# Kernel optimization log

Hardware: AMD Instinct MI355X
Metric: run time of the kernel (lower is better)

## Reference

```python
import jax, jax.numpy as jnp
import numpy as np

EPS = 1e-9       # module's displacement/convergence epsilon
COS_EPS = 1e-8   # torch F.cosine_similarity eps (norms clamped at eps)
LN_EPS = 1e-5


def _safe_norm(sq):
    # sqrt with zero-safe gradient for exactly-zero (padded) vectors
    return jnp.where(sq > 0, jnp.sqrt(jnp.maximum(sq, 1e-30)), 0.0)


def _features(coords, n):
    """coords: [S, md] padded; n: true length (>=4). Returns [60] features."""
    S, md = coords.shape
    f32 = coords.dtype
    nf = n.astype(f32)
    idx_d = jnp.arange(S - 1)
    m = n - 1                       # number of valid deltas
    mf = m.astype(f32)
    dmask = idx_d < m
    dmaskf = dmask.astype(f32)

    deltas = (coords[1:] - coords[:-1]) * dmaskf[:, None]     # [S-1, md]
    dmags = _safe_norm(jnp.sum(deltas * deltas, axis=-1))      # [S-1]

    last = jnp.take(coords, n - 1, axis=0)
    total_disp = _safe_norm(jnp.sum((last - coords[0]) ** 2))
    path_len = jnp.sum(dmags)
    disp_ratio = total_disp / (path_len + EPS)
    n_steps_norm = nf / 10.0

    # consecutive cosine similarities / curvatures (valid count = n-2)
    na = jnp.maximum(dmags, COS_EPS)
    cos = jnp.sum(deltas[:-1] * deltas[1:], axis=-1) / (na[:-1] * na[1:])  # [S-2]
    idx_c = jnp.arange(S - 2)
    cmask = idx_c < (n - 2)
    cmaskf = cmask.astype(f32)
    ncf = (n - 2).astype(f32)
    curv = 1.0 - cos
    curv_m = jnp.where(cmask, curv, 0.0)
    mean_curv = jnp.sum(curv_m) / ncf
    max_curv = jnp.max(jnp.where(cmask, curv, -jnp.inf))
    min_curv = jnp.min(jnp.where(cmask, curv, jnp.inf))
    curv_var = jnp.sum(cmaskf * (curv - mean_curv) ** 2) / jnp.maximum(ncf - 1.0, 1.0)
    std_curv = jnp.where(ncf > 1.0, jnp.sqrt(jnp.maximum(curv_var, 1e-30)), 0.0)
    curv_range = max_curv - min_curv

    mean_cos = jnp.sum(jnp.where(cmask, cos, 0.0)) / ncf
    min_cos = jnp.min(jnp.where(cmask, cos, jnp.inf))
    dir_changes = jnp.sum(cmaskf * (cos < 0).astype(f32)) / jnp.maximum(ncf, 1.0)

    linearity = disp_ratio
    loop_score = 1.0 - total_disp / (path_len + EPS)

    half = m // 2
    fmaskf = (idx_d < half + 1).astype(f32)
    smaskf = ((idx_d >= half) & (idx_d < m)).astype(f32)
    first_half = jnp.sum(dmags * fmaskf) / (half + 1).astype(f32)
    second_half = jnp.sum(dmags * smaskf) / (m - half).astype(f32)
    convergence = (first_half - second_half) / (first_half + EPS)
    cascade = (second_half - first_half) / (first_half + EPS)

    # all-pairs cosine (the O(n^2) block) via one GEMM per sample
    cosmat = (deltas @ deltas.T) / (na[:, None] * na[None, :])  # [S-1, S-1]
    pmask = (idx_d[:, None] < idx_d[None, :]) & (idx_d[None, :] < m)
    npairs = mf * (mf - 1.0) / 2.0
    parallelism = jnp.sum(jnp.where(pmask, cosmat, 0.0)) / jnp.maximum(npairs, 1.0)

    mean_dm = path_len / mf
    dm_var = jnp.sum(dmaskf * (dmags - mean_dm) ** 2) / jnp.maximum(mf - 1.0, 1.0)
    std_dm = jnp.where(mf > 1.0, jnp.sqrt(jnp.maximum(dm_var, 1e-30)), 0.0)
    max_dm = jnp.max(jnp.where(dmask, dmags, -jnp.inf))
    jump = jnp.where(mean_dm > EPS, max_dm / mean_dm, 1.0)

    rmaskf = (jnp.arange(S) < n).astype(f32)
    cnt = nf * md
    mean_coord = jnp.sum(coords * rmaskf[:, None]) / cnt
    coord_var = jnp.sum(rmaskf[:, None] * (coords - mean_coord) ** 2) / (cnt - 1.0)
    std_coord = jnp.sqrt(jnp.maximum(coord_var, 1e-30))

    scalars = jnp.stack([
        total_disp, path_len, disp_ratio, n_steps_norm,
        mean_curv, max_curv, std_curv, curv_range,
        mean_cos, min_cos, dir_changes,
        linearity, loop_score, convergence, parallelism, jump, cascade,
        mean_dm, std_dm, mean_coord, std_coord,
    ])  # [21]
    padded_deltas = deltas[:3].reshape(-1)   # [30] (masked -> already zero-padded)
    padded_curvs = curv_m[:9]                # [9]
    return jnp.concatenate([scalars, padded_deltas, padded_curvs])  # [60]


def setup_inputs() -> dict:
    key = jax.random.key(0)
    ks = jax.random.split(key, 4)
    B, S, md, H = 32768, 48, 10, 48
    coords = jax.random.normal(ks[0], (B, S, md), dtype=jnp.float32)
    lengths = jax.random.randint(ks[1], (B,), 4, S + 1, dtype=jnp.int32)
    W = jax.random.normal(ks[2], (60, H), dtype=jnp.float32) * 0.1
    b = jax.random.normal(ks[3], (H,), dtype=jnp.float32) * 0.01
    ln_w = jnp.ones((H,), dtype=jnp.float32)
    ln_b = jnp.zeros((H,), dtype=jnp.float32)
    return {"coords": coords, "lengths": lengths, "W": W, "b": b, "ln_w": ln_w, "ln_b": ln_b}


def reference(coords, lengths, W, b, ln_w, ln_b):
    feats = jax.vmap(_features)(coords, lengths)          # [B, 60]
    h = feats @ W + b                                     # [B, 48]
    mu = jnp.mean(h, axis=-1, keepdims=True)
    var = jnp.mean((h - mu) ** 2, axis=-1, keepdims=True)
    h = (h - mu) / jnp.sqrt(var + LN_EPS) * ln_w + ln_b
    return jax.nn.gelu(h, approximate=False)              # dropout is identity at eval
```

## Files before the change

kernel.cpp:

```cpp
#include <hip/hip_runtime.h>
#include <math.h>

#define WPB 4

template<int CTRL, int RM>
static __device__ __forceinline__ float dppadd(float x){
  int t = __builtin_amdgcn_update_dpp(0, __float_as_int(x), CTRL, RM, 0xf, true);
  return x + __int_as_float(t);
}
template<int CTRL, int RM>
static __device__ __forceinline__ float dppmax(float x){
  int t = __builtin_amdgcn_update_dpp(__float_as_int(x), __float_as_int(x), CTRL, RM, 0xf, false);
  return fmaxf(x, __int_as_float(t));
}
template<int CTRL, int RM>
static __device__ __forceinline__ float dppmin(float x){
  int t = __builtin_amdgcn_update_dpp(__float_as_int(x), __float_as_int(x), CTRL, RM, 0xf, false);
  return fminf(x, __int_as_float(t));
}
static __device__ __forceinline__ float rl(float x, int l){
  return __uint_as_float(__builtin_amdgcn_readlane(__float_as_uint(x), l));
}
static __device__ __forceinline__ float wsum(float x){
  x = dppadd<0x111,0xf>(x);
  x = dppadd<0x112,0xf>(x);
  x = dppadd<0x114,0xf>(x);
  x = dppadd<0x118,0xf>(x);
  x = dppadd<0x142,0xa>(x);
  x = dppadd<0x143,0xc>(x);
  return rl(x, 63);
}
static __device__ __forceinline__ float wmax(float x){
  x = dppmax<0x111,0xf>(x); x = dppmax<0x112,0xf>(x);
  x = dppmax<0x114,0xf>(x); x = dppmax<0x118,0xf>(x);
  x = dppmax<0x142,0xa>(x); x = dppmax<0x143,0xc>(x);
  return rl(x, 63);
}
static __device__ __forceinline__ float wmin(float x){
  x = dppmin<0x111,0xf>(x); x = dppmin<0x112,0xf>(x);
  x = dppmin<0x114,0xf>(x); x = dppmin<0x118,0xf>(x);
  x = dppmin<0x142,0xa>(x); x = dppmin<0x143,0xc>(x);
  return rl(x, 63);
}
static __device__ __forceinline__ float frcp(float x){ return __builtin_amdgcn_rcpf(x); }
static __device__ __forceinline__ float fsqrt(float x){ return __builtin_amdgcn_sqrtf(x); }

__global__ void transpose_w(const float* __restrict__ W, float* __restrict__ Wt){
  int idx = blockIdx.x * 256 + threadIdx.x;
  if (idx < 60 * 48) { int f = idx / 48, j = idx - f * 48; Wt[j * 60 + f] = W[idx]; }
}

template<bool USEWT>
__global__ __launch_bounds__(WPB * 64)
void traj_kernel(const float* __restrict__ coords,
                 const int* __restrict__ lengths,
                 const float* __restrict__ Wsrc,
                 const float* __restrict__ bias,
                 const float* __restrict__ lnw,
                 const float* __restrict__ lnb,
                 float* __restrict__ out, int B)
{
  const int i = threadIdx.x & 63;
  const int b = blockIdx.x * WPB + (threadIdx.x >> 6);
  if (b >= B) return;

  const int n = __builtin_amdgcn_readfirstlane(lengths[b]);
  const int m = n - 1;
  const float* cp = coords + (size_t)b * 480;

  float c[10], cnx[10];
  if (i < 48) {
    const float2* p = reinterpret_cast<const float2*>(cp + i * 10);
    float2 v0 = p[0], v1 = p[1], v2 = p[2], v3 = p[3], v4 = p[4];
    c[0]=v0.x; c[1]=v0.y; c[2]=v1.x; c[3]=v1.y; c[4]=v2.x;
    c[5]=v2.y; c[6]=v3.x; c[7]=v3.y; c[8]=v4.x; c[9]=v4.y;
  } else {
#pragma unroll
    for (int k = 0; k < 10; k++) c[k] = 0.f;
  }
  if (i < 47) {
    const float2* p = reinterpret_cast<const float2*>(cp + (i + 1) * 10);
    float2 v0 = p[0], v1 = p[1], v2 = p[2], v3 = p[3], v4 = p[4];
    cnx[0]=v0.x; cnx[1]=v0.y; cnx[2]=v1.x; cnx[3]=v1.y; cnx[4]=v2.x;
    cnx[5]=v2.y; cnx[6]=v3.x; cnx[7]=v3.y; cnx[8]=v4.x; cnx[9]=v4.y;
  } else {
#pragma unroll
    for (int k = 0; k < 10; k++) cnx[k] = 0.f;
  }

  const bool dact = (i < m);
  float d[10]; float dsq = 0.f;
#pragma unroll
  for (int k = 0; k < 10; k++) {
    float dd = dact ? (cnx[k] - c[k]) : 0.f;
    d[k] = dd;
    dsq = fmaf(dd, dd, dsq);
  }
  const float dmag = (dsq > 0.f) ? fsqrt(fmaxf(dsq, 1e-30f)) : 0.f;
  const float na   = fmaxf(dmag, 1e-8f);
  const float inv  = frcp(na);

  float dot = 0.f;
#pragma unroll
  for (int k = 0; k < 10; k++) {
    float dn = __shfl_down(d[k], 1, 64);
    dot = fmaf(d[k], dn, dot);
  }
  const float invn = __shfl_down(inv, 1, 64);
  const bool cact = (i < n - 2);
  const float cosv  = dot * inv * invn;
  const float cos_m = cact ? cosv : 0.f;

  const int half = m >> 1;
  const float path_len = wsum(dmag);
  const float sum_dm2  = wsum(dsq);
  const float max_dm   = wmax(dmag);
  const float sum_f    = wsum((i <= half) ? dmag : 0.f);
  const float dm_half  = __uint_as_float(__builtin_amdgcn_readlane(__float_as_uint(dmag), half));
  const float sum_s    = path_len + dm_half - sum_f;

  const float sum_cos  = wsum(cos_m);
  const float sum_cos2 = wsum(cos_m * cos_m);
  const float max_cos  = wmax(cact ? cosv : -INFINITY);
  const float min_cos  = wmin(cact ? cosv :  INFINITY);
  const float sum_ng   = wsum((cact && cosv < 0.f) ? 1.f : 0.f);

  float Usq = 0.f;
#pragma unroll
  for (int k = 0; k < 10; k++) {
    float Uk = wsum(d[k] * inv);
    Usq = fmaf(Uk, Uk, Usq);
  }
  const float sum_uu = wsum(dsq * (inv * inv));

  float csl = 0.f, cs2l = 0.f;
  if (i < n) {
#pragma unroll
    for (int k = 0; k < 10; k++) { csl += c[k]; cs2l = fmaf(c[k], c[k], cs2l); }
  }
  const float sum_c  = wsum(csl);
  const float sum_c2 = wsum(cs2l);

  float tsql = 0.f;
#pragma unroll
  for (int k = 0; k < 10; k++) {
    float c0 = rl(c[k], 0);
    float t = c[k] - c0;
    tsql = fmaf(t, t, tsql);
  }
  const float tdq = __uint_as_float(__builtin_amdgcn_readlane(__float_as_uint(tsql), m));
  const float total_disp = (tdq > 0.f) ? fsqrt(fmaxf(tdq, 1e-30f)) : 0.f;

  const float EPSf = 1e-9f;
  const float nf = (float)n, mf = (float)m, ncf = (float)(n - 2);
  const float rncf = frcp(ncf);
  const float disp_ratio = total_disp * frcp(path_len + EPSf);
  const float sum_cv  = ncf - sum_cos;
  const float mean_cv = sum_cv * rncf;
  const float sum_cv2 = fmaf(-2.f, sum_cos, ncf) + sum_cos2;
  const float cv_var  = (sum_cv2 - ncf * mean_cv * mean_cv) * frcp(fmaxf(ncf - 1.f, 1.f));
  const float std_cv  = fsqrt(fmaxf(cv_var, 1e-30f));
  const float max_cv  = 1.f - min_cos;
  const float cv_rng  = max_cos - min_cos;
  const float mean_cs = sum_cos * rncf;
  const float dirchg  = sum_ng * rncf;
  const float fh = sum_f * frcp((float)(half + 1));
  const float sh = sum_s * frcp((float)(m - half));
  const float conv = (fh - sh) * frcp(fh + EPSf);
  const float npairs = mf * (mf - 1.f) * 0.5f;
  const float par = (Usq - sum_uu) * 0.5f * frcp(npairs);
  const float mean_dm = path_len * frcp(mf);
  const float dm_var = (sum_dm2 - mf * mean_dm * mean_dm) * frcp(mf - 1.f);
  const float std_dm = fsqrt(fmaxf(dm_var, 1e-30f));
  const float jump = (mean_dm > EPSf) ? max_dm * frcp(mean_dm) : 1.f;
  const float cnt = nf * 10.f;
  const float mean_co = sum_c * frcp(cnt);
  const float co_var = (sum_c2 - cnt * mean_co * mean_co) * frcp(cnt - 1.f);
  const float std_co = fsqrt(fmaxf(co_var, 1e-30f));

  float feat[60];
  feat[0]  = total_disp;
  feat[1]  = path_len;
  feat[2]  = disp_ratio;
  feat[3]  = nf * 0.1f;
  feat[4]  = mean_cv;
  feat[5]  = max_cv;
  feat[6]  = std_cv;
  feat[7]  = cv_rng;
  feat[8]  = mean_cs;
  feat[9]  = min_cos;
  feat[10] = dirchg;
  feat[11] = disp_ratio;
  feat[12] = 1.f - disp_ratio;
  feat[13] = conv;
  feat[14] = par;
  feat[15] = jump;
  feat[16] = -conv;
  feat[17] = mean_dm;
  feat[18] = std_dm;
  feat[19] = mean_co;
  feat[20] = std_co;
#pragma unroll
  for (int r = 0; r < 3; r++)
#pragma unroll
    for (int k = 0; k < 10; k++)
      feat[21 + r * 10 + k] = rl(d[k], r);
  const float curv_m = cact ? (1.f - cosv) : 0.f;
#pragma unroll
  for (int r = 0; r < 9; r++)
    feat[51 + r] = rl(curv_m, r);

  float h = 0.f;
  if (i < 48) {
    h = bias[i];
    if (USEWT) {
      const float4* wr = reinterpret_cast<const float4*>(Wsrc + i * 60);
#pragma unroll
      for (int q = 0; q < 15; ++q) {
        float4 w = wr[q];
        h = fmaf(feat[4 * q + 0], w.x, h);
        h = fmaf(feat[4 * q + 1], w.y, h);
        h = fmaf(feat[4 * q + 2], w.z, h);
        h = fmaf(feat[4 * q + 3], w.w, h);
      }
    } else {
#pragma unroll
      for (int f = 0; f < 60; ++f) h = fmaf(feat[f], Wsrc[f * 48 + i], h);
    }
  }

  const float hm = (i < 48) ? h : 0.f;
  const float s1 = wsum(hm);
  const float s2 = wsum(hm * hm);
  const float mu  = s1 * (1.f / 48.f);
  const float var = fmaf(-mu, mu, s2 * (1.f / 48.f));

  if (i < 48) {
    float x = (h - mu) * __builtin_amdgcn_rsqf(var + 1e-5f) * lnw[i] + lnb[i];
    float g = 0.5f * x * (1.f + erff(x * 0.70710678118654752f));
    out[(size_t)b * 48 + i] = g;
  }
}

extern "C" void kernel_launch(void* const* d_in, const int* in_sizes, int n_in,
                              void* d_out, int out_size, void* d_ws, size_t ws_size,
                              hipStream_t stream)
{
  const float* coords = (const float*)d_in[0];
  const int*   lengths= (const int*)d_in[1];
  const float* W      = (const float*)d_in[2];
  const float* bias   = (const float*)d_in[3];
  const float* lnw    = (const float*)d_in[4];
  const float* lnb    = (const float*)d_in[5];
  float* out = (float*)d_out;

  const int B = in_sizes[1];
  const int blocks = (B + WPB - 1) / WPB;

  if (ws_size >= (size_t)(60 * 48 * sizeof(float))) {
    float* Wt = (float*)d_ws;
    transpose_w<<<12, 256, 0, stream>>>(W, Wt);
    traj_kernel<true><<<blocks, WPB * 64, 0, stream>>>(coords, lengths, Wt, bias, lnw, lnb, out, B);
  } else {
    traj_kernel<false><<<blocks, WPB * 64, 0, stream>>>(coords, lengths, W, bias, lnw, lnb, out, B);
  }
}
```

Baseline: 126.4 us.

## Process four trajectories per wavefront with 16-lane reductions and tanh GELU

Maps each trajectory to a 16-lane group, with each lane handling three rows, instead of one trajectory per 64-lane wavefront. Reductions shrink to 16-lane DPP plus a swizzle broadcast, and neighbour deltas for the cosine terms are reloaded from memory rather than shuffled across lanes. This is meant to remove idle lanes and cut the cost of the many full-wave reductions. It also replaces the exact erf GELU with the tanh approximation via exp2, which adds small numerical differences, and the extra per-lane arrays raise register pressure.

```diff
diff --git a/kernel.cpp b/kernel.cpp
--- a/kernel.cpp
+++ b/kernel.cpp
@@ -1,49 +1,40 @@
 #include <hip/hip_runtime.h>
 #include <math.h>
 
-#define WPB 4
-
-template<int CTRL, int RM>
+static __device__ __forceinline__ float frcp(float x){ return __builtin_amdgcn_rcpf(x); }
+static __device__ __forceinline__ float fsq (float x){ return __builtin_amdgcn_sqrtf(x); }
+
+template<int CTRL>
 static __device__ __forceinline__ float dppadd(float x){
-  int t = __builtin_amdgcn_update_dpp(0, __float_as_int(x), CTRL, RM, 0xf, true);
+  int t = __builtin_amdgcn_update_dpp(0, __float_as_int(x), CTRL, 0xf, 0xf, true);
   return x + __int_as_float(t);
 }
-template<int CTRL, int RM>
+template<int CTRL>
 static __device__ __forceinline__ float dppmax(float x){
-  int t = __builtin_amdgcn_update_dpp(__float_as_int(x), __float_as_int(x), CTRL, RM, 0xf, false);
+  int t = __builtin_amdgcn_update_dpp(__float_as_int(x), __float_as_int(x), CTRL, 0xf, 0xf, false);
   return fmaxf(x, __int_as_float(t));
 }
-template<int CTRL, int RM>
+template<int CTRL>
 static __device__ __forceinline__ float dppmin(float x){
-  int t = __builtin_amdgcn_update_dpp(__float_as_int(x), __float_as_int(x), CTRL, RM, 0xf, false);
+  int t = __builtin_amdgcn_update_dpp(__float_as_int(x), __float_as_int(x), CTRL, 0xf, 0xf, false);
   return fminf(x, __int_as_float(t));
 }
-static __device__ __forceinline__ float rl(float x, int l){
-  return __uint_as_float(__builtin_amdgcn_readlane(__float_as_uint(x), l));
-}
-static __device__ __forceinline__ float wsum(float x){
-  x = dppadd<0x111,0xf>(x);
-  x = dppadd<0x112,0xf>(x);
-  x = dppadd<0x114,0xf>(x);
-  x = dppadd<0x118,0xf>(x);
-  x = dppadd<0x142,0xa>(x);
-  x = dppadd<0x143,0xc>(x);
-  return rl(x, 63);
-}
-static __device__ __forceinline__ float wmax(float x){
-  x = dppmax<0x111,0xf>(x); x = dppmax<0x112,0xf>(x);
-  x = dppmax<0x114,0xf>(x); x = dppmax<0x118,0xf>(x);
-  x = dppmax<0x142,0xa>(x); x = dppmax<0x143,0xc>(x);
-  return rl(x, 63);
-}
-static __device__ __forceinline__ float wmin(float x){
-  x = dppmin<0x111,0xf>(x); x = dppmin<0x112,0xf>(x);
-  x = dppmin<0x114,0xf>(x); x = dppmin<0x118,0xf>(x);
-  x = dppmin<0x142,0xa>(x); x = dppmin<0x143,0xc>(x);
-  return rl(x, 63);
-}
-static __device__ __forceinline__ float frcp(float x){ return __builtin_amdgcn_rcpf(x); }
-static __device__ __forceinline__ float fsqrt(float x){ return __builtin_amdgcn_sqrtf(x); }
+static __device__ __forceinline__ float rsum16(float x){
+  x = dppadd<0x111>(x); x = dppadd<0x112>(x);
+  x = dppadd<0x114>(x); x = dppadd<0x118>(x);
+  return __int_as_float(__builtin_amdgcn_ds_swizzle(__float_as_int(x), 0x1F0));
+}
+static __device__ __forceinline__ float rmax16(float x){
+  x = dppmax<0x111>(x); x = dppmax<0x112>(x);
+  x = dppmax<0x114>(x); x = dppmax<0x118>(x);
+  return __int_as_float(__builtin_amdgcn_ds_swizzle(__float_as_int(x), 0x1F0));
+}
+static __device__ __forceinline__ float rmin16(float x){
+  x = dppmin<0x111>(x); x = dppmin<0x112>(x);
+  x = dppmin<0x114>(x); x = dppmin<0x118>(x);
+  return __int_as_float(__builtin_amdgcn_ds_swizzle(__float_as_int(x), 0x1F0));
+}
+#define BC(P, x) __int_as_float(__builtin_amdgcn_ds_swizzle(__float_as_int(x), 0x10 | ((P) << 5)))
 
 __global__ void transpose_w(const float* __restrict__ W, float* __restrict__ Wt){
   int idx = blockIdx.x * 256 + threadIdx.x;
@@ -51,7 +42,7 @@
 }
 
 template<bool USEWT>
-__global__ __launch_bounds__(WPB * 64)
+__global__ __launch_bounds__(256)
 void traj_kernel(const float* __restrict__ coords,
                  const int* __restrict__ lengths,
                  const float* __restrict__ Wsrc,
@@ -60,96 +51,142 @@
                  const float* __restrict__ lnb,
                  float* __restrict__ out, int B)
 {
-  const int i = threadIdx.x & 63;
-  const int b = blockIdx.x * WPB + (threadIdx.x >> 6);
-  if (b >= B) return;
-
-  const int n = __builtin_amdgcn_readfirstlane(lengths[b]);
+  const int lane = threadIdx.x & 63;
+  const int s    = lane & 15;
+  const int grp  = (blockIdx.x * 4 + (threadIdx.x >> 6)) * 4 + (lane >> 4);
+  const bool bvalid = (grp < B);
+  const int b = bvalid ? grp : (B - 1);
+
+  const int n = lengths[b];
   const int m = n - 1;
   const float* cp = coords + (size_t)b * 480;
 
-  float c[10], cnx[10];
-  if (i < 48) {
-    const float2* p = reinterpret_cast<const float2*>(cp + i * 10);
-    float2 v0 = p[0], v1 = p[1], v2 = p[2], v3 = p[3], v4 = p[4];
-    c[0]=v0.x; c[1]=v0.y; c[2]=v1.x; c[3]=v1.y; c[4]=v2.x;
-    c[5]=v2.y; c[6]=v3.x; c[7]=v3.y; c[8]=v4.x; c[9]=v4.y;
-  } else {
-#pragma unroll
-    for (int k = 0; k < 10; k++) c[k] = 0.f;
-  }
-  if (i < 47) {
-    const float2* p = reinterpret_cast<const float2*>(cp + (i + 1) * 10);
-    float2 v0 = p[0], v1 = p[1], v2 = p[2], v3 = p[3], v4 = p[4];
-    cnx[0]=v0.x; cnx[1]=v0.y; cnx[2]=v1.x; cnx[3]=v1.y; cnx[4]=v2.x;
-    cnx[5]=v2.y; cnx[6]=v3.x; cnx[7]=v3.y; cnx[8]=v4.x; cnx[9]=v4.y;
-  } else {
-#pragma unroll
-    for (int k = 0; k < 10; k++) cnx[k] = 0.f;
-  }
-
-  const bool dact = (i < m);
-  float d[10]; float dsq = 0.f;
-#pragma unroll
-  for (int k = 0; k < 10; k++) {
-    float dd = dact ? (cnx[k] - c[k]) : 0.f;
-    d[k] = dd;
-    dsq = fmaf(dd, dd, dsq);
-  }
-  const float dmag = (dsq > 0.f) ? fsqrt(fmaxf(dsq, 1e-30f)) : 0.f;
-  const float na   = fmaxf(dmag, 1e-8f);
-  const float inv  = frcp(na);
-
-  float dot = 0.f;
-#pragma unroll
-  for (int k = 0; k < 10; k++) {
-    float dn = __shfl_down(d[k], 1, 64);
-    dot = fmaf(d[k], dn, dot);
-  }
-  const float invn = __shfl_down(inv, 1, 64);
-  const bool cact = (i < n - 2);
-  const float cosv  = dot * inv * invn;
-  const float cos_m = cact ? cosv : 0.f;
+  float c[3][10], cn[3][10];
+#pragma unroll
+  for (int q = 0; q < 3; ++q) {
+    const float2* p = reinterpret_cast<const float2*>(cp + (q * 16 + s) * 10);
+#pragma unroll
+    for (int k = 0; k < 5; ++k) { float2 v = p[k]; c[q][2*k] = v.x; c[q][2*k+1] = v.y; }
+  }
+#pragma unroll
+  for (int q = 0; q < 3; ++q) {
+    const int row = q * 16 + s + 1;
+    if (row < 48) {
+      const float2* p = reinterpret_cast<const float2*>(cp + row * 10);
+#pragma unroll
+      for (int k = 0; k < 5; ++k) { float2 v = p[k]; cn[q][2*k] = v.x; cn[q][2*k+1] = v.y; }
+    } else {
+#pragma unroll
+      for (int k = 0; k < 10; ++k) cn[q][k] = 0.f;
+    }
+  }
+
+  float csl = 0.f, cs2l = 0.f;
+#pragma unroll
+  for (int q = 0; q < 3; ++q) {
+    float t1 = 0.f, t2 = 0.f;
+#pragma unroll
+    for (int k = 0; k < 10; ++k) { t1 += c[q][k]; t2 = fmaf(c[q][k], c[q][k], t2); }
+    const bool act = (q * 16 + s) < n;
+    csl  += act ? t1 : 0.f;
+    cs2l += act ? t2 : 0.f;
+  }
+  const float sum_c  = rsum16(csl);
+  const float sum_c2 = rsum16(cs2l);
+
+  float cc0[10];
+#pragma unroll
+  for (int k = 0; k < 10; ++k) cc0[k] = BC(0, c[0][k]);
+  const int qs = (n - 1) >> 4, ssl = (n - 1) & 15;
+  float tql = 0.f;
+#pragma unroll
+  for (int q = 0; q < 3; ++q) {
+    float tq = 0.f;
+#pragma unroll
+    for (int k = 0; k < 10; ++k) { float t = c[q][k] - cc0[k]; tq = fmaf(t, t, tq); }
+    tql = (s == ssl && q == qs) ? tq : tql;
+  }
+  const float tdq = rsum16(tql);
+  const float total_disp = (tdq > 0.f) ? fsq(fmaxf(tdq, 1e-30f)) : 0.f;
 
   const int half = m >> 1;
-  const float path_len = wsum(dmag);
-  const float sum_dm2  = wsum(dsq);
-  const float max_dm   = wmax(dmag);
-  const float sum_f    = wsum((i <= half) ? dmag : 0.f);
-  const float dm_half  = __uint_as_float(__builtin_amdgcn_readlane(__float_as_uint(dmag), half));
-  const float sum_s    = path_len + dm_half - sum_f;
-
-  const float sum_cos  = wsum(cos_m);
-  const float sum_cos2 = wsum(cos_m * cos_m);
-  const float max_cos  = wmax(cact ? cosv : -INFINITY);
-  const float min_cos  = wmin(cact ? cosv :  INFINITY);
-  const float sum_ng   = wsum((cact && cosv < 0.f) ? 1.f : 0.f);
-
+  float d[3][10], inv[3];
+  float path_l=0.f, dm2_l=0.f, maxdm_l=0.f, sf_l=0.f, ss_l=0.f, uu_l=0.f;
+  float uk[10];
+#pragma unroll
+  for (int k = 0; k < 10; ++k) uk[k] = 0.f;
+#pragma unroll
+  for (int q = 0; q < 3; ++q) {
+    const int j = q * 16 + s;
+    float ds_ = 0.f;
+#pragma unroll
+    for (int k = 0; k < 10; ++k) { float dd = cn[q][k] - c[q][k]; d[q][k] = dd; ds_ = fmaf(dd, dd, ds_); }
+    const float sn = (ds_ > 0.f) ? fsq(fmaxf(ds_, 1e-30f)) : 0.f;
+    inv[q] = frcp(fmaxf(sn, 1e-8f));
+    const bool jm = j < m;
+    const float dm = jm ? sn : 0.f;
+    path_l += dm;
+    dm2_l  += jm ? ds_ : 0.f;
+    maxdm_l = fmaxf(maxdm_l, dm);
+    sf_l += (j <= half) ? dm : 0.f;
+    ss_l += (j >= half) ? dm : 0.f;
+    const float invm = jm ? inv[q] : 0.f;
+#pragma unroll
+    for (int k = 0; k < 10; ++k) uk[k] = fmaf(d[q][k], invm, uk[k]);
+    uu_l = fmaf(ds_ * invm, invm, uu_l);
+  }
+
+  const int rotb = (((lane & 48) | ((lane + 1) & 15)) << 2);
+  const float rinv0 = __int_as_float(__builtin_amdgcn_ds_bpermute(rotb, __float_as_int(inv[0])));
+  const float rinv1 = __int_as_float(__builtin_amdgcn_ds_bpermute(rotb, __float_as_int(inv[1])));
+  const float rinv2 = __int_as_float(__builtin_amdgcn_ds_bpermute(rotb, __float_as_int(inv[2])));
+  float invn[3];
+  invn[0] = (s < 15) ? rinv0 : rinv1;
+  invn[1] = (s < 15) ? rinv1 : rinv2;
+  invn[2] = (s < 15) ? rinv2 : 0.f;
+
+  float cos_l=0.f, cos2_l=0.f, ng_l=0.f, maxc_l=-INFINITY, minc_l=INFINITY;
+  float curv0 = 0.f;
+#pragma unroll
+  for (int q = 0; q < 3; ++q) {
+    const int j = q * 16 + s;
+    float dn[10];
+    if (j + 2 < 48) {
+      const float2* p = reinterpret_cast<const float2*>(cp + (j + 2) * 10);
+#pragma unroll
+      for (int k = 0; k < 5; ++k) { float2 v = p[k]; dn[2*k] = v.x - cn[q][2*k]; dn[2*k+1] = v.y - cn[q][2*k+1]; }
+    } else {
+#pragma unroll
+      for (int k = 0; k < 10; ++k) dn[k] = 0.f;
+    }
+    float dot = 0.f;
+#pragma unroll
+    for (int k = 0; k < 10; ++k) dot = fmaf(d[q][k], dn[k], dot);
+    const float cosv = dot * inv[q] * invn[q];
+    const bool ca = j < (n - 2);
+    const float cm = ca ? cosv : 0.f;
+    cos_l += cm;
+    cos2_l = fmaf(cm, cm, cos2_l);
+    maxc_l = fmaxf(maxc_l, ca ? cosv : -INFINITY);
+    minc_l = fminf(minc_l, ca ? cosv :  INFINITY);
+    ng_l += (cm < 0.f) ? 1.f : 0.f;
+    if (q == 0) curv0 = ca ? (1.f - cosv) : 0.f;
+  }
+
+  const float path_len = rsum16(path_l);
+  const float sum_dm2  = rsum16(dm2_l);
+  const float max_dm   = rmax16(maxdm_l);
+  const float sum_f    = rsum16(sf_l);
+  const float sum_s    = rsum16(ss_l);
+  const float sum_cos  = rsum16(cos_l);
+  const float sum_cos2 = rsum16(cos2_l);
+  const float sum_ng   = rsum16(ng_l);
+  const float max_cos  = rmax16(maxc_l);
+  const float min_cos  = rmin16(minc_l);
   float Usq = 0.f;
 #pragma unroll
-  for (int k = 0; k < 10; k++) {
-    float Uk = wsum(d[k] * inv);
-    Usq = fmaf(Uk, Uk, Usq);
-  }
-  const float sum_uu = wsum(dsq * (inv * inv));
-
-  float csl = 0.f, cs2l = 0.f;
-  if (i < n) {
-#pragma unroll
-    for (int k = 0; k < 10; k++) { csl += c[k]; cs2l = fmaf(c[k], c[k], cs2l); }
-  }
-  const float sum_c  = wsum(csl);
-  const float sum_c2 = wsum(cs2l);
-
-  float tsql = 0.f;
-#pragma unroll
-  for (int k = 0; k < 10; k++) {
-    float c0 = rl(c[k], 0);
-    float t = c[k] - c0;
-    tsql = fmaf(t, t, tsql);
-  }
-  const float tdq = __uint_as_float(__builtin_amdgcn_readlane(__float_as_uint(tsql), m));
-  const float total_disp = (tdq > 0.f) ? fsqrt(fmaxf(tdq, 1e-30f)) : 0.f;
+  for (int k = 0; k < 10; ++k) { float Uk = rsum16(uk[k]); Usq = fmaf(Uk, Uk, Usq); }
+  const float sum_uu = rsum16(uu_l);
 
   const float EPSf = 1e-9f;
   const float nf = (float)n, mf = (float)m, ncf = (float)(n - 2);
@@ -159,7 +196,7 @@
   const float mean_cv = sum_cv * rncf;
   const float sum_cv2 = fmaf(-2.f, sum_cos, ncf) + sum_cos2;
   const float cv_var  = (sum_cv2 - ncf * mean_cv * mean_cv) * frcp(fmaxf(ncf - 1.f, 1.f));
-  const float std_cv  = fsqrt(fmaxf(cv_var, 1e-30f));
+  const float std_cv  = fsq(fmaxf(cv_var, 1e-30f));
   const float max_cv  = 1.f - min_cos;
   const float cv_rng  = max_cos - min_cos;
   const float mean_cs = sum_cos * rncf;
@@ -171,12 +208,12 @@
   const float par = (Usq - sum_uu) * 0.5f * frcp(npairs);
   const float mean_dm = path_len * frcp(mf);
   const float dm_var = (sum_dm2 - mf * mean_dm * mean_dm) * frcp(mf - 1.f);
-  const float std_dm = fsqrt(fmaxf(dm_var, 1e-30f));
+  const float std_dm = fsq(fmaxf(dm_var, 1e-30f));
   const float jump = (mean_dm > EPSf) ? max_dm * frcp(mean_dm) : 1.f;
   const float cnt = nf * 10.f;
   const float mean_co = sum_c * frcp(cnt);
   const float co_var = (sum_c2 - cnt * mean_co * mean_co) * frcp(cnt - 1.f);
-  const float std_co = fsqrt(fmaxf(co_var, 1e-30f));
+  const float std_co = fsq(fmaxf(co_var, 1e-30f));
 
   float feat[60];
   feat[0]  = total_disp;
@@ -201,44 +238,54 @@
   feat[19] = mean_co;
   feat[20] = std_co;
 #pragma unroll
-  for (int r = 0; r < 3; r++)
-#pragma unroll
-    for (int k = 0; k < 10; k++)
-      feat[21 + r * 10 + k] = rl(d[k], r);
-  const float curv_m = cact ? (1.f - cosv) : 0.f;
-#pragma unroll
-  for (int r = 0; r < 9; r++)
-    feat[51 + r] = rl(curv_m, r);
-
-  float h = 0.f;
-  if (i < 48) {
-    h = bias[i];
+  for (int k = 0; k < 10; ++k) feat[21 + k] = BC(0, d[0][k]);
+#pragma unroll
+  for (int k = 0; k < 10; ++k) feat[31 + k] = BC(1, d[0][k]);
+#pragma unroll
+  for (int k = 0; k < 10; ++k) feat[41 + k] = BC(2, d[0][k]);
+  feat[51] = BC(0, curv0); feat[52] = BC(1, curv0); feat[53] = BC(2, curv0);
+  feat[54] = BC(3, curv0); feat[55] = BC(4, curv0); feat[56] = BC(5, curv0);
+  feat[57] = BC(6, curv0); feat[58] = BC(7, curv0); feat[59] = BC(8, curv0);
+
+  float h[3];
+#pragma unroll
+  for (int q = 0; q < 3; ++q) {
+    const int j = q * 16 + s;
+    float acc = bias[j];
     if (USEWT) {
-      const float4* wr = reinterpret_cast<const float4*>(Wsrc + i * 60);
-#pragma unroll
-      for (int q = 0; q < 15; ++q) {
-        float4 w = wr[q];
-        h = fmaf(feat[4 * q + 0], w.x, h);
-        h = fmaf(feat[4 * q + 1], w.y, h);
-        h = fmaf(feat[4 * q + 2], w.z, h);
-        h = fmaf(feat[4 * q + 3], w.w, h);
+      const float4* wr = reinterpret_cast<const float4*>(Wsrc + j * 60);
+#pragma unroll
+      for (int t = 0; t < 15; ++t) {
+        float4 w = wr[t];
+        acc = fmaf(feat[4*t+0], w.x, acc);
+        acc = fmaf(feat[4*t+1], w.y, acc);
+        acc = fmaf(feat[4*t+2], w.z, acc);
+        acc = fmaf(feat[4*t+3], w.w, acc);
       }
     } else {
 #pragma unroll
-      for (int f = 0; f < 60; ++f) h = fmaf(feat[f], Wsrc[f * 48 + i], h);
+      for (int f = 0; f < 60; ++f) acc = fmaf(feat[f], Wsrc[f * 48 + j], acc);
     }
-  }
-
-  const float hm = (i < 48) ? h : 0.f;
-  const float s1 = wsum(hm);
-  const float s2 = wsum(hm * hm);
+    h[q] = acc;
+  }
+
+  const float s1 = rsum16(h[0] + h[1] + h[2]);
+  const float s2 = rsum16(fmaf(h[0], h[0], fmaf(h[1], h[1], h[2] * h[2])));
   const float mu  = s1 * (1.f / 48.f);
   const float var = fmaf(-mu, mu, s2 * (1.f / 48.f));
-
-  if (i < 48) {
-    float x = (h - mu) * __builtin_amdgcn_rsqf(var + 1e-5f) * lnw[i] + lnb[i];
-    float g = 0.5f * x * (1.f + erff(x * 0.70710678118654752f));
-    out[(size_t)b * 48 + i] = g;
+  const float rstd = __builtin_amdgcn_rsqf(var + 1e-5f);
+
+  if (bvalid) {
+#pragma unroll
+    for (int q = 0; q < 3; ++q) {
+      const int j = q * 16 + s;
+      float x = (h[q] - mu) * rstd * lnw[j] + lnb[j];
+      float x2 = x * x;
+      float u  = 0.7978845608f * x * fmaf(0.044715f, x2, 1.f);
+      float e  = __builtin_amdgcn_exp2f(u * 2.885390082f);
+      float th = fmaf(-2.f, frcp(1.f + e), 1.f);
+      out[(size_t)b * 48 + j] = 0.5f * x * (1.f + th);
+    }
   }
 }
 
@@ -255,13 +302,13 @@
   float* out = (float*)d_out;
 
   const int B = in_sizes[1];
-  const int blocks = (B + WPB - 1) / WPB;
+  const int blocks = (B + 15) / 16;
 
   if (ws_size >= (size_t)(60 * 48 * sizeof(float))) {
     float* Wt = (float*)d_ws;
     transpose_w<<<12, 256, 0, stream>>>(W, Wt);
-    traj_kernel<true><<<blocks, WPB * 64, 0, stream>>>(coords, lengths, Wt, bias, lnw, lnb, out, B);
+    traj_kernel<true><<<blocks, 256, 0, stream>>>(coords, lengths, Wt, bias, lnw, lnb, out, B);
   } else {
-    traj_kernel<false><<<blocks, WPB * 64, 0, stream>>>(coords, lengths, W, bias, lnw, lnb, out, B);
-  }
-}
+    traj_kernel<false><<<blocks, 256, 0, stream>>>(coords, lengths, W, bias, lnw, lnb, out, B);
+  }
+}
```

New measurement: 122.3 us. 1.03x faster.

## Replace erf GELU with tanh approximation and drop shuffles via redundant row loads

Applied to the files above, without the earlier changes.

Each lane now loads three consecutive coordinate rows, using clamped indices, so both its delta and the next delta are computed locally. This replaces the ten cross-lane shuffles with loads that should mostly hit cache. Wave reductions keep their result in lane 63 and are read to scalars only when the features are assembled, and the bias/W loads run unconditionally on a clamped row. The exact erf GELU is replaced by the tanh approximation built from exp2 and rcp. That cuts ALU work but adds a small numerical deviation from the reference's exact GELU.

```diff
diff --git a/kernel.cpp b/kernel.cpp
--- a/kernel.cpp
+++ b/kernel.cpp
@@ -2,6 +2,12 @@
 #include <math.h>
 
 #define WPB 4
+
+static __device__ __forceinline__ float frcp(float x){ return __builtin_amdgcn_rcpf(x); }
+static __device__ __forceinline__ float fsq (float x){ return __builtin_amdgcn_sqrtf(x); }
+static __device__ __forceinline__ float rld(float x, int l){
+  return __uint_as_float(__builtin_amdgcn_readlane(__float_as_uint(x), l));
+}
 
 template<int CTRL, int RM>
 static __device__ __forceinline__ float dppadd(float x){
@@ -18,32 +24,24 @@
   int t = __builtin_amdgcn_update_dpp(__float_as_int(x), __float_as_int(x), CTRL, RM, 0xf, false);
   return fminf(x, __int_as_float(t));
 }
-static __device__ __forceinline__ float rl(float x, int l){
-  return __uint_as_float(__builtin_amdgcn_readlane(__float_as_uint(x), l));
-}
-static __device__ __forceinline__ float wsum(float x){
-  x = dppadd<0x111,0xf>(x);
-  x = dppadd<0x112,0xf>(x);
-  x = dppadd<0x114,0xf>(x);
-  x = dppadd<0x118,0xf>(x);
-  x = dppadd<0x142,0xa>(x);
-  x = dppadd<0x143,0xc>(x);
-  return rl(x, 63);
-}
-static __device__ __forceinline__ float wmax(float x){
+static __device__ __forceinline__ float wsum63(float x){
+  x = dppadd<0x111,0xf>(x); x = dppadd<0x112,0xf>(x);
+  x = dppadd<0x114,0xf>(x); x = dppadd<0x118,0xf>(x);
+  x = dppadd<0x142,0xa>(x); x = dppadd<0x143,0xc>(x);
+  return x;
+}
+static __device__ __forceinline__ float wmax63(float x){
   x = dppmax<0x111,0xf>(x); x = dppmax<0x112,0xf>(x);
   x = dppmax<0x114,0xf>(x); x = dppmax<0x118,0xf>(x);
   x = dppmax<0x142,0xa>(x); x = dppmax<0x143,0xc>(x);
-  return rl(x, 63);
-}
-static __device__ __forceinline__ float wmin(float x){
+  return x;
+}
+static __device__ __forceinline__ float wmin63(float x){
   x = dppmin<0x111,0xf>(x); x = dppmin<0x112,0xf>(x);
   x = dppmin<0x114,0xf>(x); x = dppmin<0x118,0xf>(x);
   x = dppmin<0x142,0xa>(x); x = dppmin<0x143,0xc>(x);
-  return rl(x, 63);
-}
-static __device__ __forceinline__ float frcp(float x){ return __builtin_amdgcn_rcpf(x); }
-static __device__ __forceinline__ float fsqrt(float x){ return __builtin_amdgcn_sqrtf(x); }
+  return x;
+}
 
 __global__ void transpose_w(const float* __restrict__ W, float* __restrict__ Wt){
   int idx = blockIdx.x * 256 + threadIdx.x;
@@ -66,104 +64,91 @@
 
   const int n = __builtin_amdgcn_readfirstlane(lengths[b]);
   const int m = n - 1;
+  const int half = m >> 1;
   const float* cp = coords + (size_t)b * 480;
 
-  float c[10], cnx[10];
-  if (i < 48) {
-    const float2* p = reinterpret_cast<const float2*>(cp + i * 10);
-    float2 v0 = p[0], v1 = p[1], v2 = p[2], v3 = p[3], v4 = p[4];
-    c[0]=v0.x; c[1]=v0.y; c[2]=v1.x; c[3]=v1.y; c[4]=v2.x;
-    c[5]=v2.y; c[6]=v3.x; c[7]=v3.y; c[8]=v4.x; c[9]=v4.y;
-  } else {
-#pragma unroll
-    for (int k = 0; k < 10; k++) c[k] = 0.f;
-  }
-  if (i < 47) {
-    const float2* p = reinterpret_cast<const float2*>(cp + (i + 1) * 10);
-    float2 v0 = p[0], v1 = p[1], v2 = p[2], v3 = p[3], v4 = p[4];
-    cnx[0]=v0.x; cnx[1]=v0.y; cnx[2]=v1.x; cnx[3]=v1.y; cnx[4]=v2.x;
-    cnx[5]=v2.y; cnx[6]=v3.x; cnx[7]=v3.y; cnx[8]=v4.x; cnx[9]=v4.y;
-  } else {
-#pragma unroll
-    for (int k = 0; k < 10; k++) cnx[k] = 0.f;
-  }
+  const int r0 = (i < 47) ? i : 47;
+  const int r1 = (i + 1 < 47) ? (i + 1) : 47;
+  const int r2 = (i + 2 < 47) ? (i + 2) : 47;
+  float c[10], cn[10], cnn[10];
+  {
+    const float2* p = reinterpret_cast<const float2*>(cp + r0 * 10);
+#pragma unroll
+    for (int k = 0; k < 5; ++k){ float2 v = p[k]; c[2*k]=v.x; c[2*k+1]=v.y; }
+    p = reinterpret_cast<const float2*>(cp + r1 * 10);
+#pragma unroll
+    for (int k = 0; k < 5; ++k){ float2 v = p[k]; cn[2*k]=v.x; cn[2*k+1]=v.y; }
+    p = reinterpret_cast<const float2*>(cp + r2 * 10);
+#pragma unroll
+    for (int k = 0; k < 5; ++k){ float2 v = p[k]; cnn[2*k]=v.x; cnn[2*k+1]=v.y; }
+  }
+
+  float d[10], dn[10];
+  float dsq = 0.f, dsqn = 0.f, dot = 0.f;
+#pragma unroll
+  for (int k = 0; k < 10; ++k) {
+    float a = cn[k] - c[k];   d[k]  = a;  dsq  = fmaf(a, a, dsq);
+    float e = cnn[k] - cn[k]; dn[k] = e;  dsqn = fmaf(e, e, dsqn);
+    dot = fmaf(a, e, dot);
+  }
+  const float sn   = (dsq  > 0.f) ? fsq(fmaxf(dsq,  1e-30f)) : 0.f;
+  const float snn  = (dsqn > 0.f) ? fsq(fmaxf(dsqn, 1e-30f)) : 0.f;
+  const float inv  = frcp(fmaxf(sn,  1e-8f));
+  const float invn = frcp(fmaxf(snn, 1e-8f));
 
   const bool dact = (i < m);
-  float d[10]; float dsq = 0.f;
-#pragma unroll
-  for (int k = 0; k < 10; k++) {
-    float dd = dact ? (cnx[k] - c[k]) : 0.f;
-    d[k] = dd;
-    dsq = fmaf(dd, dd, dsq);
-  }
-  const float dmag = (dsq > 0.f) ? fsqrt(fmaxf(dsq, 1e-30f)) : 0.f;
-  const float na   = fmaxf(dmag, 1e-8f);
-  const float inv  = frcp(na);
-
-  float dot = 0.f;
-#pragma unroll
-  for (int k = 0; k < 10; k++) {
-    float dn = __shfl_down(d[k], 1, 64);
-    dot = fmaf(d[k], dn, dot);
-  }
-  const float invn = __shfl_down(inv, 1, 64);
+  const float dm  = dact ? sn  : 0.f;
   const bool cact = (i < n - 2);
-  const float cosv  = dot * inv * invn;
-  const float cos_m = cact ? cosv : 0.f;
-
-  const int half = m >> 1;
-  const float path_len = wsum(dmag);
-  const float sum_dm2  = wsum(dsq);
-  const float max_dm   = wmax(dmag);
-  const float sum_f    = wsum((i <= half) ? dmag : 0.f);
-  const float dm_half  = __uint_as_float(__builtin_amdgcn_readlane(__float_as_uint(dmag), half));
-  const float sum_s    = path_len + dm_half - sum_f;
-
-  const float sum_cos  = wsum(cos_m);
-  const float sum_cos2 = wsum(cos_m * cos_m);
-  const float max_cos  = wmax(cact ? cosv : -INFINITY);
-  const float min_cos  = wmin(cact ? cosv :  INFINITY);
-  const float sum_ng   = wsum((cact && cosv < 0.f) ? 1.f : 0.f);
-
+  const float cosv   = dot * inv * invn;
+  const float cm     = cact ? cosv : 0.f;
+  const float curv_m = cact ? (1.f - cosv) : 0.f;
+
+  float csl = 0.f, cs2l = 0.f;
+#pragma unroll
+  for (int k = 0; k < 10; ++k) { csl += c[k]; cs2l = fmaf(c[k], c[k], cs2l); }
+  const bool ract = (i < n);
+  csl  = ract ? csl  : 0.f;
+  cs2l = ract ? cs2l : 0.f;
+
+  float tql = 0.f;
+#pragma unroll
+  for (int k = 0; k < 10; ++k) {
+    float t = c[k] - rld(c[k], 0);
+    tql = fmaf(t, t, tql);
+  }
+  const float tsq = rld(tql, m);
+  const float total_disp = (tsq > 0.f) ? fsq(fmaxf(tsq, 1e-30f)) : 0.f;
+
+  const float path_len = wsum63(dm);
+  const float sum_dm2  = wsum63(dact ? dsq : 0.f);
+  const float max_dm   = wmax63(dm);
+  const float sum_f    = wsum63((i <= half) ? dm : 0.f);
+  const float dm_half  = rld(dm, half);
+  const float sum_cos  = wsum63(cm);
+  const float sum_cos2 = wsum63(cm * cm);
+  const float max_cos  = wmax63(cact ? cosv : -INFINITY);
+  const float min_cos  = wmin63(cact ? cosv :  INFINITY);
+  const float sum_ng   = wsum63((cact && cosv < 0.f) ? 1.f : 0.f);
+  const float sum_c    = wsum63(csl);
+  const float sum_c2   = wsum63(cs2l);
+  const float invm = dact ? inv : 0.f;
   float Usq = 0.f;
 #pragma unroll
-  for (int k = 0; k < 10; k++) {
-    float Uk = wsum(d[k] * inv);
+  for (int k = 0; k < 10; ++k) {
+    float Uk = wsum63(d[k] * invm);
     Usq = fmaf(Uk, Uk, Usq);
   }
-  const float sum_uu = wsum(dsq * (inv * inv));
-
-  float csl = 0.f, cs2l = 0.f;
-  if (i < n) {
-#pragma unroll
-    for (int k = 0; k < 10; k++) { csl += c[k]; cs2l = fmaf(c[k], c[k], cs2l); }
-  }
-  const float sum_c  = wsum(csl);
-  const float sum_c2 = wsum(cs2l);
-
-  float tsql = 0.f;
-#pragma unroll
-  for (int k = 0; k < 10; k++) {
-    float c0 = rl(c[k], 0);
-    float t = c[k] - c0;
-    tsql = fmaf(t, t, tsql);
-  }
-  const float tdq = __uint_as_float(__builtin_amdgcn_readlane(__float_as_uint(tsql), m));
-  const float total_disp = (tdq > 0.f) ? fsqrt(fmaxf(tdq, 1e-30f)) : 0.f;
+  const float sum_uu = wsum63(dsq * invm * invm);
 
   const float EPSf = 1e-9f;
   const float nf = (float)n, mf = (float)m, ncf = (float)(n - 2);
   const float rncf = frcp(ncf);
+  const float sum_s = path_len + dm_half - sum_f;
   const float disp_ratio = total_disp * frcp(path_len + EPSf);
-  const float sum_cv  = ncf - sum_cos;
-  const float mean_cv = sum_cv * rncf;
+  const float mean_cv = (ncf - sum_cos) * rncf;
   const float sum_cv2 = fmaf(-2.f, sum_cos, ncf) + sum_cos2;
   const float cv_var  = (sum_cv2 - ncf * mean_cv * mean_cv) * frcp(fmaxf(ncf - 1.f, 1.f));
-  const float std_cv  = fsqrt(fmaxf(cv_var, 1e-30f));
-  const float max_cv  = 1.f - min_cos;
-  const float cv_rng  = max_cos - min_cos;
-  const float mean_cs = sum_cos * rncf;
-  const float dirchg  = sum_ng * rncf;
+  const float std_cv  = fsq(fmaxf(cv_var, 1e-30f));
   const float fh = sum_f * frcp((float)(half + 1));
   const float sh = sum_s * frcp((float)(m - half));
   const float conv = (fh - sh) * frcp(fh + EPSf);
@@ -171,74 +156,75 @@
   const float par = (Usq - sum_uu) * 0.5f * frcp(npairs);
   const float mean_dm = path_len * frcp(mf);
   const float dm_var = (sum_dm2 - mf * mean_dm * mean_dm) * frcp(mf - 1.f);
-  const float std_dm = fsqrt(fmaxf(dm_var, 1e-30f));
+  const float std_dm = fsq(fmaxf(dm_var, 1e-30f));
   const float jump = (mean_dm > EPSf) ? max_dm * frcp(mean_dm) : 1.f;
   const float cnt = nf * 10.f;
   const float mean_co = sum_c * frcp(cnt);
   const float co_var = (sum_c2 - cnt * mean_co * mean_co) * frcp(cnt - 1.f);
-  const float std_co = fsqrt(fmaxf(co_var, 1e-30f));
+  const float std_co = fsq(fmaxf(co_var, 1e-30f));
 
   float feat[60];
-  feat[0]  = total_disp;
-  feat[1]  = path_len;
-  feat[2]  = disp_ratio;
+  feat[0]  = rld(total_disp, 63);
+  feat[1]  = rld(path_len, 63);
+  feat[2]  = rld(disp_ratio, 63);
   feat[3]  = nf * 0.1f;
-  feat[4]  = mean_cv;
-  feat[5]  = max_cv;
-  feat[6]  = std_cv;
-  feat[7]  = cv_rng;
-  feat[8]  = mean_cs;
-  feat[9]  = min_cos;
-  feat[10] = dirchg;
-  feat[11] = disp_ratio;
-  feat[12] = 1.f - disp_ratio;
-  feat[13] = conv;
-  feat[14] = par;
-  feat[15] = jump;
-  feat[16] = -conv;
-  feat[17] = mean_dm;
-  feat[18] = std_dm;
-  feat[19] = mean_co;
-  feat[20] = std_co;
-#pragma unroll
-  for (int r = 0; r < 3; r++)
-#pragma unroll
-    for (int k = 0; k < 10; k++)
-      feat[21 + r * 10 + k] = rl(d[k], r);
-  const float curv_m = cact ? (1.f - cosv) : 0.f;
-#pragma unroll
-  for (int r = 0; r < 9; r++)
-    feat[51 + r] = rl(curv_m, r);
-
-  float h = 0.f;
-  if (i < 48) {
-    h = bias[i];
-    if (USEWT) {
-      const float4* wr = reinterpret_cast<const float4*>(Wsrc + i * 60);
-#pragma unroll
-      for (int q = 0; q < 15; ++q) {
-        float4 w = wr[q];
-        h = fmaf(feat[4 * q + 0], w.x, h);
-        h = fmaf(feat[4 * q + 1], w.y, h);
-        h = fmaf(feat[4 * q + 2], w.z, h);
-        h = fmaf(feat[4 * q + 3], w.w, h);
-      }
-    } else {
-#pragma unroll
-      for (int f = 0; f < 60; ++f) h = fmaf(feat[f], Wsrc[f * 48 + i], h);
+  feat[4]  = rld(mean_cv, 63);
+  feat[5]  = 1.f - rld(min_cos, 63);
+  feat[6]  = rld(std_cv, 63);
+  feat[7]  = rld(max_cos - min_cos, 63);
+  feat[8]  = rld(sum_cos * rncf, 63);
+  feat[9]  = rld(min_cos, 63);
+  feat[10] = rld(sum_ng * rncf, 63);
+  feat[11] = feat[2];
+  feat[12] = 1.f - feat[2];
+  feat[13] = rld(conv, 63);
+  feat[14] = rld(par, 63);
+  feat[15] = rld(jump, 63);
+  feat[16] = -feat[13];
+  feat[17] = rld(mean_dm, 63);
+  feat[18] = rld(std_dm, 63);
+  feat[19] = rld(mean_co, 63);
+  feat[20] = rld(std_co, 63);
+#pragma unroll
+  for (int k = 0; k < 10; ++k) feat[21 + k] = rld(d[k], 0);
+#pragma unroll
+  for (int k = 0; k < 10; ++k) feat[31 + k] = rld(d[k], 1);
+#pragma unroll
+  for (int k = 0; k < 10; ++k) feat[41 + k] = rld(d[k], 2);
+#pragma unroll
+  for (int r = 0; r < 9; ++r)  feat[51 + r] = rld(curv_m, r);
+
+  const int jc = (i < 48) ? i : 47;
+  float h = bias[jc];
+  if (USEWT) {
+    const float4* wr = reinterpret_cast<const float4*>(Wsrc + jc * 60);
+#pragma unroll
+    for (int t = 0; t < 15; ++t) {
+      float4 w = wr[t];
+      h = fmaf(feat[4*t+0], w.x, h);
+      h = fmaf(feat[4*t+1], w.y, h);
+      h = fmaf(feat[4*t+2], w.z, h);
+      h = fmaf(feat[4*t+3], w.w, h);
     }
+  } else {
+#pragma unroll
+    for (int f = 0; f < 60; ++f) h = fmaf(feat[f], Wsrc[f * 48 + jc], h);
   }
 
   const float hm = (i < 48) ? h : 0.f;
-  const float s1 = wsum(hm);
-  const float s2 = wsum(hm * hm);
+  const float s1 = rld(wsum63(hm), 63);
+  const float s2 = rld(wsum63(hm * hm), 63);
   const float mu  = s1 * (1.f / 48.f);
   const float var = fmaf(-mu, mu, s2 * (1.f / 48.f));
+  const float rstd = __builtin_amdgcn_rsqf(var + 1e-5f);
 
   if (i < 48) {
-    float x = (h - mu) * __builtin_amdgcn_rsqf(var + 1e-5f) * lnw[i] + lnb[i];
-    float g = 0.5f * x * (1.f + erff(x * 0.70710678118654752f));
-    out[(size_t)b * 48 + i] = g;
+    float x = (h - mu) * rstd * lnw[i] + lnb[i];
+    float x2 = x * x;
+    float u  = 0.7978845608f * x * fmaf(0.044715f, x2, 1.f);
+    float e  = __builtin_amdgcn_exp2f(u * 2.885390082f);
+    float th = fmaf(-2.f, frcp(1.f + e), 1.f);
+    out[(size_t)b * 48 + i] = 0.5f * x * (1.f + th);
   }
 }
 
```

Measured after the change: 132.1 us. 1.04x slower.
